# Kernel optimization log

Hardware: AMD Instinct MI355X
Metric: run time of the kernel (lower is better)

## Reference

```python
import jax, jax.numpy as jnp
import numpy as np

N = 50000      # nodes
E = 1_600_000  # edges
F = 64         # input_shape
FE = 1         # input_shape_edge
G = 512        # graphs in batch


def _uniform(k, shape, size):
    b = 1.0 / np.sqrt(size)
    return jax.random.uniform(k, shape, jnp.float32, -b, b)


def setup_inputs() -> dict:
    key = jax.random.key(0)
    ks = jax.random.split(key, 24)
    inp = {
        "x": jax.random.normal(ks[0], (N, F), jnp.float32),
        "edge_index": jax.random.randint(ks[1], (2, E), 0, N),
        "edge_attr": jax.random.uniform(ks[2], (E, FE), jnp.float32),
        "batch": jnp.sort(jax.random.randint(ks[3], (N,), 0, G)),
    }
    # conv layers: (in, out); reset_parameters uses uniform(1/sqrt(in_channels)) for all three weights
    specs = [("c1", F, 16), ("c2", 16, 32), ("c1e", F, 16), ("c2e", 16, 32)]
    i = 4
    for name, cin, cout in specs:
        inp[f"{name}_fc"] = _uniform(ks[i], (cout, cin), cin); i += 1
        inp[f"{name}_e"] = _uniform(ks[i], (FE, FE), cin); i += 1
        inp[f"{name}_a"] = _uniform(ks[i], (1, 2 * cout + FE), cin); i += 1
    inp["fc1_w"] = _uniform(ks[i], (128, 64), 64); i += 1
    inp["fc1_b"] = _uniform(ks[i], (128,), 64); i += 1
    inp["fc2_w"] = _uniform(ks[i], (1, 128), 128); i += 1
    inp["fc2_b"] = _uniform(ks[i], (1,), 128); i += 1
    return inp


def _conv(x, row, col, ea, wfc, we, wa):
    xc = x[col] @ wfc.T            # [E, out] gather + linear
    xr = x[row] @ wfc.T            # [E, out]
    ed = ea @ we.T                 # [E, FE]
    a = jnp.concatenate([xr, xc, ed], axis=1) @ wa.T  # [E, 1]
    # faithful to torch source: softmax over dim=1 of a size-1 dim -> all ones
    a = jax.nn.softmax(jax.nn.leaky_relu(a), axis=1)
    return jax.ops.segment_sum(a * xc, row, num_segments=x.shape[0])  # [N, out]


def reference(x, edge_index, edge_attr, batch,
              c1_fc, c1_e, c1_a, c2_fc, c2_e, c2_a,
              c1e_fc, c1e_e, c1e_a, c2e_fc, c2e_e, c2e_a,
              fc1_w, fc1_b, fc2_w, fc2_b):
    row, col = edge_index[0], edge_index[1]
    h = jax.nn.relu(_conv(x, row, col, edge_attr, c1_fc, c1_e, c1_a))
    h = jax.nn.relu(_conv(h, row, col, edge_attr, c2_fc, c2_e, c2_a))
    he = jax.nn.relu(_conv(x, row, col, edge_attr, c1e_fc, c1e_e, c1e_a))
    he = jax.nn.relu(_conv(he, row, col, edge_attr, c2e_fc, c2e_e, c2e_a))
    cnt = jax.ops.segment_sum(jnp.ones((x.shape[0],), jnp.float32), batch, num_segments=G)
    cnt = jnp.maximum(cnt, 1.0)[:, None]
    pool = lambda z: jax.ops.segment_sum(z, batch, num_segments=G) / cnt  # scatter_mean
    g = jnp.concatenate([pool(h), pool(he)], axis=1)  # [G, 64]
    g = jax.nn.relu(g @ fc1_w.T + fc1_b)
    # dropout: eval mode (identity)
    return g @ fc2_w.T + fc2_b  # [G, 1]
```

## Files before the change

kernel.cpp:

```cpp
#include <hip/hip_runtime.h>
#include <hip/hip_fp16.h>

#define NN 50000
#define NE 1600000
#define NG 512
#define RB 98
#define NB 511
#define NNP (NB * RB)
#define SEGCAP 512
#define CAP 72
#define PBLK 200
#define EPB (NE / PBLK)
#define G1_BLOCKS ((NN * 16 + 511) / 512)
#define ZWORDS (NB * 8 + NG * 64)

union H8 { uint4 u; __half2 h[4]; };
union H4 { uint2 u; __half2 h[2]; };

__global__ __launch_bounds__(256) void zero_k(int* __restrict__ p) {
    int i = blockIdx.x * 256 + threadIdx.x;
    for (; i < ZWORDS; i += 64 * 256) p[i] = 0;
}

__global__ __launch_bounds__(512) void part_gemm1(const int* __restrict__ ei,
                                                  int* __restrict__ bcur,
                                                  unsigned int* __restrict__ bucket,
                                                  const float* __restrict__ x,
                                                  const float* __restrict__ w_a,
                                                  const float* __restrict__ w_b,
                                                  __half* __restrict__ y) {
    __shared__ union {
        struct {
            int lc[NB];
            unsigned short rank[EPB];
        } p;
        float Wt[64][33];
    } sm;
    int tid = threadIdx.x;
    if (blockIdx.x < PBLK) {
        int xcd = blockIdx.x & 7;
        for (int i = tid; i < NB; i += 512) sm.p.lc[i] = 0;
        __syncthreads();
        int e0 = blockIdx.x * EPB;
        const int4* row4 = reinterpret_cast<const int4*>(ei + e0);
        const int4* col4 = reinterpret_cast<const int4*>(ei + NE + e0);
        for (int i0 = tid * 4; i0 < EPB; i0 += 2048) {
            int4 r = row4[i0 >> 2];
            sm.p.rank[i0 + 0] = (unsigned short)atomicAdd(&sm.p.lc[r.x / RB], 1);
            sm.p.rank[i0 + 1] = (unsigned short)atomicAdd(&sm.p.lc[r.y / RB], 1);
            sm.p.rank[i0 + 2] = (unsigned short)atomicAdd(&sm.p.lc[r.z / RB], 1);
            sm.p.rank[i0 + 3] = (unsigned short)atomicAdd(&sm.p.lc[r.w / RB], 1);
        }
        __syncthreads();
        if (tid < NB) sm.p.lc[tid] = atomicAdd(&bcur[tid * 8 + xcd], sm.p.lc[tid]);
        __syncthreads();
        for (int i0 = tid * 4; i0 < EPB; i0 += 2048) {
            int4 r = row4[i0 >> 2];
            int4 c = col4[i0 >> 2];
#pragma unroll
            for (int j = 0; j < 4; ++j) {
                int row = (j == 0) ? r.x : (j == 1) ? r.y : (j == 2) ? r.z : r.w;
                int col = (j == 0) ? c.x : (j == 1) ? c.y : (j == 2) ? c.z : c.w;
                int g = row / RB, lr = row - g * RB;
                int pos = sm.p.lc[g] + (int)sm.p.rank[i0 + j];
                if (pos < SEGCAP)
                    bucket[(g * 8 + xcd) * SEGCAP + pos] = ((unsigned)lr << 16) | (unsigned)col;
            }
        }
    } else {
        for (int i = tid; i < 16 * 64; i += 512) {
            sm.Wt[i & 63][i >> 6] = w_a[i];
            sm.Wt[i & 63][16 + (i >> 6)] = w_b[i];
        }
        __syncthreads();
        int idx = (blockIdx.x - PBLK) * 512 + tid;
        if (idx < NN * 16) {
            int n = idx >> 4, q = idx & 15;
            const float4* xr = reinterpret_cast<const float4*>(x + n * 64);
            float acc0 = 0.f, acc1 = 0.f;
#pragma unroll
            for (int k4 = 0; k4 < 16; ++k4) {
                float4 a = xr[k4];
                acc0 += a.x * sm.Wt[4 * k4 + 0][q] + a.y * sm.Wt[4 * k4 + 1][q] +
                        a.z * sm.Wt[4 * k4 + 2][q] + a.w * sm.Wt[4 * k4 + 3][q];
                acc1 += a.x * sm.Wt[4 * k4 + 0][q + 16] + a.y * sm.Wt[4 * k4 + 1][q + 16] +
                        a.z * sm.Wt[4 * k4 + 2][q + 16] + a.w * sm.Wt[4 * k4 + 3][q + 16];
            }
            y[n * 32 + q] = __float2half_rn(acc0);
            y[n * 32 + q + 16] = __float2half_rn(acc1);
        }
    }
}

__global__ __launch_bounds__(512) void fillgather1(const int* __restrict__ bcur,
                                                   const unsigned int* __restrict__ bucket,
                                                   int* __restrict__ deg,
                                                   unsigned short* __restrict__ cols,
                                                   const __half* __restrict__ y,
                                                   __half* __restrict__ h) {
    __shared__ __align__(16) unsigned short slab[RB * CAP];
    __shared__ int cur[RB];
    __shared__ int scnt[8];
    int tid = threadIdx.x, b = blockIdx.x;
    if (tid < RB) cur[tid] = 0;
    if (tid >= 128 && tid < 136) scnt[tid - 128] = min(bcur[b * 8 + (tid - 128)], SEGCAP);
    __syncthreads();
    const uint4* bseg = reinterpret_cast<const uint4*>(bucket + (size_t)b * 8 * SEGCAP);
#pragma unroll
    for (int k = 0; k < 2; ++k) {
        int f = tid * 4 + k * 2048;
        int seg = f >> 9, pos = f & 511;
        int cnt = scnt[seg];
        if (pos >= cnt) continue;
        uint4 v4 = bseg[f >> 2];
        int lim = cnt - pos;
        {
            unsigned v = v4.x; int lr = v >> 16;
            int p = atomicAdd(&cur[lr], 1);
            if (p < CAP) slab[lr * CAP + p] = (unsigned short)(v & 0xffffu);
        }
        if (lim > 1) {
            unsigned v = v4.y; int lr = v >> 16;
            int p = atomicAdd(&cur[lr], 1);
            if (p < CAP) slab[lr * CAP + p] = (unsigned short)(v & 0xffffu);
        }
        if (lim > 2) {
            unsigned v = v4.z; int lr = v >> 16;
            int p = atomicAdd(&cur[lr], 1);
            if (p < CAP) slab[lr * CAP + p] = (unsigned short)(v & 0xffffu);
        }
        if (lim > 3) {
            unsigned v = v4.w; int lr = v >> 16;
            int p = atomicAdd(&cur[lr], 1);
            if (p < CAP) slab[lr * CAP + p] = (unsigned short)(v & 0xffffu);
        }
    }
    __syncthreads();
    if (tid < RB) {
        int d = min(cur[tid], CAP);
        cur[tid] = d;
        deg[b * RB + tid] = d;
    }
    {
        const uint4* src = reinterpret_cast<const uint4*>(slab);
        uint4* dst = reinterpret_cast<uint4*>(cols) + (size_t)b * (RB * CAP / 8);
        for (int i = tid; i < RB * CAP / 8; i += 512) dst[i] = src[i];
    }
    __syncthreads();
    const uint2* y2 = reinterpret_cast<const uint2*>(y);
#pragma unroll 1
    for (int rp = 0; rp < 2; ++rp) {
        int r = rp * 64 + (tid >> 3);
        if (r >= RB) continue;
        int n = b * RB + r;
        if (n >= NN) continue;
        int d = cur[r], g = tid & 7;
        const unsigned short* c = &slab[r * CAP];
        float acc[4] = {0.f, 0.f, 0.f, 0.f};
        int i = 0;
        for (; i + 3 < d; i += 4) {
            H4 v0, v1, v2, v3;
            v0.u = y2[(int)c[i] * 8 + g];
            v1.u = y2[(int)c[i + 1] * 8 + g];
            v2.u = y2[(int)c[i + 2] * 8 + g];
            v3.u = y2[(int)c[i + 3] * 8 + g];
#pragma unroll
            for (int j = 0; j < 2; ++j) {
                float2 f0 = __half22float2(v0.h[j]);
                float2 f1 = __half22float2(v1.h[j]);
                float2 f2 = __half22float2(v2.h[j]);
                float2 f3 = __half22float2(v3.h[j]);
                acc[2 * j] += (f0.x + f1.x) + (f2.x + f3.x);
                acc[2 * j + 1] += (f0.y + f1.y) + (f2.y + f3.y);
            }
        }
        for (; i < d; ++i) {
            H4 v0;
            v0.u = y2[(int)c[i] * 8 + g];
#pragma unroll
            for (int j = 0; j < 2; ++j) {
                float2 f0 = __half22float2(v0.h[j]);
                acc[2 * j] += f0.x;
                acc[2 * j + 1] += f0.y;
            }
        }
        H4 o;
#pragma unroll
        for (int j = 0; j < 2; ++j) {
            float2 f = {fmaxf(acc[2 * j], 0.f), fmaxf(acc[2 * j + 1], 0.f)};
            o.h[j] = __float22half2_rn(f);
        }
        reinterpret_cast<uint2*>(h)[n * 8 + g] = o.u;
    }
}

__global__ __launch_bounds__(512) void gatherD(const int* __restrict__ deg,
                                               const unsigned short* __restrict__ cols,
                                               const __half* __restrict__ h,
                                               const float* __restrict__ w_a,
                                               const float* __restrict__ w_b,
                                               const int* __restrict__ batch,
                                               float* __restrict__ gpool) {
    __shared__ float U[64][33];
    __shared__ float W2[64][17];
    __shared__ int bl[64];
    int tid = threadIdx.x;
    int n0 = blockIdx.x * 64;
    for (int i = tid; i < 32 * 16; i += 512) W2[i >> 4][i & 15] = w_a[i];
    for (int i = tid; i < 32 * 16; i += 512) W2[32 + (i >> 4)][i & 15] = w_b[i];
    if (tid < 64) bl[tid] = (n0 + tid < NN) ? batch[n0 + tid] : -1;
    int nl = tid >> 3, g = tid & 7;
    int n = n0 + nl;
    float acc[4] = {0.f, 0.f, 0.f, 0.f};
    if (n < NN) {
        int d = deg[n];
        const unsigned short* cs = cols + (size_t)n * CAP;
        const unsigned int* cp = reinterpret_cast<const unsigned int*>(cs);
        const uint2* h2 = reinterpret_cast<const uint2*>(h);
        int i = 0;
        for (; i + 3 < d; i += 4) {
            unsigned int cc0 = cp[i >> 1], cc1 = cp[(i >> 1) + 1];
            H4 v0, v1, v2, v3;
            v0.u = h2[(cc0 & 0xffffu) * 8 + g];
            v1.u = h2[(cc0 >> 16) * 8 + g];
            v2.u = h2[(cc1 & 0xffffu) * 8 + g];
            v3.u = h2[(cc1 >> 16) * 8 + g];
#pragma unroll
            for (int j = 0; j < 2; ++j) {
                float2 f0 = __half22float2(v0.h[j]);
                float2 f1 = __half22float2(v1.h[j]);
                float2 f2 = __half22float2(v2.h[j]);
                float2 f3 = __half22float2(v3.h[j]);
                acc[2 * j] += (f0.x + f1.x) + (f2.x + f3.x);
                acc[2 * j + 1] += (f0.y + f1.y) + (f2.y + f3.y);
            }
        }
        for (; i < d; ++i) {
            H4 v0;
            v0.u = h2[(int)cs[i] * 8 + g];
#pragma unroll
            for (int j = 0; j < 2; ++j) {
                float2 f0 = __half22float2(v0.h[j]);
                acc[2 * j] += f0.x;
                acc[2 * j + 1] += f0.y;
            }
        }
    }
#pragma unroll
    for (int j = 0; j < 4; ++j) U[nl][g * 4 + j] = acc[j];
    __syncthreads();
    int o = tid & 63, w = tid >> 6;
    int ub = (o < 32) ? 0 : 16;
    int curg = -1;
    float sum = 0.f;
#pragma unroll 1
    for (int r = w; r < 64; r += 8) {
        if (n0 + r >= NN) break;
        float a = 0.f;
#pragma unroll
        for (int k = 0; k < 16; ++k) a += U[r][ub + k] * W2[o][k];
        a = fmaxf(a, 0.f);
        int gb = bl[r];
        if (gb != curg) {
            if (curg >= 0) atomicAdd(&gpool[curg * 64 + o], sum);
            curg = gb;
            sum = a;
        } else {
            sum += a;
        }
    }
    if (curg >= 0) atomicAdd(&gpool[curg * 64 + o], sum);
}

__global__ __launch_bounds__(128) void mlp_k(const float* __restrict__ gpool,
                                             const int* __restrict__ batch,
                                             const float* __restrict__ fc1_w,
                                             const float* __restrict__ fc1_b,
                                             const float* __restrict__ fc2_w,
                                             const float* __restrict__ fc2_b,
                                             float* __restrict__ out) {
    int b = blockIdx.x, tid = threadIdx.x;
    int lo = 0, hi = NN;
    while (lo < hi) { int m = (lo + hi) >> 1; if (batch[m] < b) lo = m + 1; else hi = m; }
    int start = lo;
    lo = start; hi = NN;
    while (lo < hi) { int m = (lo + hi) >> 1; if (batch[m] < b + 1) lo = m + 1; else hi = m; }
    int end = lo;
    float inv = 1.f / (float)max(end - start, 1);

    __shared__ float gvec[64];
    if (tid < 64) gvec[tid] = gpool[b * 64 + tid] * inv;
    __syncthreads();

    float hj = fc1_b[tid];
    const float* w = fc1_w + tid * 64;
#pragma unroll
    for (int k = 0; k < 64; ++k) hj += gvec[k] * w[k];
    hj = fmaxf(hj, 0.f);
    __shared__ float red[128];
    red[tid] = hj * fc2_w[tid];
    __syncthreads();
    for (int s = 64; s > 0; s >>= 1) {
        if (tid < s) red[tid] += red[tid + s];
        __syncthreads();
    }
    if (tid == 0) out[b] = red[0] + fc2_b[0];
}

static inline size_t align256(size_t v) { return (v + 255) & ~(size_t)255; }

extern "C" void kernel_launch(void* const* d_in, const int* in_sizes, int n_in,
                              void* d_out, int out_size, void* d_ws, size_t ws_size,
                              hipStream_t stream) {
    const float* x      = (const float*)d_in[0];
    const int*   ei     = (const int*)d_in[1];
    const int*   batch  = (const int*)d_in[3];
    const float* c1_fc  = (const float*)d_in[4];
    const float* c2_fc  = (const float*)d_in[7];
    const float* c1e_fc = (const float*)d_in[10];
    const float* c2e_fc = (const float*)d_in[13];
    const float* fc1_w  = (const float*)d_in[16];
    const float* fc1_b  = (const float*)d_in[17];
    const float* fc2_w  = (const float*)d_in[18];
    const float* fc2_b  = (const float*)d_in[19];
    float* out = (float*)d_out;

    char* base = (char*)d_ws;
    size_t off = 0;
    int* bcur            = (int*)(base + off);            off += sizeof(int) * NB * 8;
    float* gpool         = (float*)(base + off);          off += sizeof(float) * NG * 64;
    off = align256(off);
    unsigned int* bucket = (unsigned int*)(base + off);   off += sizeof(unsigned int) * (size_t)NB * 8 * SEGCAP;
    off = align256(off);
    unsigned short* cols = (unsigned short*)(base + off); off += sizeof(unsigned short) * (size_t)NNP * CAP;
    off = align256(off);
    int* deg             = (int*)(base + off);            off += sizeof(int) * NNP;
    off = align256(off);
    __half* y            = (__half*)(base + off);         off += sizeof(__half) * (size_t)NN * 32;
    off = align256(off);
    __half* h            = (__half*)(base + off);         off += sizeof(__half) * (size_t)NN * 32;

    zero_k<<<64, 256, 0, stream>>>(bcur);
    part_gemm1<<<PBLK + G1_BLOCKS, 512, 0, stream>>>(ei, bcur, bucket, x, c1_fc, c1e_fc, y);
    fillgather1<<<NB, 512, 0, stream>>>(bcur, bucket, deg, cols, y, h);
    gatherD<<<(NN + 63) / 64, 512, 0, stream>>>(deg, cols, h, c2_fc, c2e_fc, batch, gpool);
    mlp_k<<<NG, 128, 0, stream>>>(gpool, batch, fc1_w, fc1_b, fc2_w, fc2_b, out);
}
```

Before: 81.73 us.

## Fuse fill/gather and second gather into one cooperative kernel with grid sync

Merges the fillgather1 and gatherD kernels into a single cooperative kernel that keeps the per-block column slab in shared memory across a grid-wide barrier. This removes the global write and re-read of the cols and deg arrays and one kernel launch. In exchange it needs all 511 blocks of 512 threads to be co-resident for the grid sync, adds the sync's cost, and uses more shared memory per block, which may limit occupancy.

```diff
diff --git a/kernel.cpp b/kernel.cpp
--- a/kernel.cpp
+++ b/kernel.cpp
@@ -1,12 +1,13 @@
 #include <hip/hip_runtime.h>
 #include <hip/hip_fp16.h>
+#include <hip/hip_cooperative_groups.h>
+namespace cg = cooperative_groups;
 
 #define NN 50000
 #define NE 1600000
 #define NG 512
 #define RB 98
 #define NB 511
-#define NNP (NB * RB)
 #define SEGCAP 512
 #define CAP 72
 #define PBLK 200
@@ -14,7 +15,6 @@
 #define G1_BLOCKS ((NN * 16 + 511) / 512)
 #define ZWORDS (NB * 8 + NG * 64)
 
-union H8 { uint4 u; __half2 h[4]; };
 union H4 { uint2 u; __half2 h[2]; };
 
 __global__ __launch_bounds__(256) void zero_k(int* __restrict__ p) {
@@ -92,16 +92,23 @@
     }
 }
 
-__global__ __launch_bounds__(512) void fillgather1(const int* __restrict__ bcur,
-                                                   const unsigned int* __restrict__ bucket,
-                                                   int* __restrict__ deg,
-                                                   unsigned short* __restrict__ cols,
-                                                   const __half* __restrict__ y,
-                                                   __half* __restrict__ h) {
+__global__ __launch_bounds__(512) void fuse_bcd(const int* __restrict__ bcur,
+                                                const unsigned int* __restrict__ bucket,
+                                                const __half* __restrict__ y,
+                                                __half* __restrict__ h,
+                                                const float* __restrict__ w_a,
+                                                const float* __restrict__ w_b,
+                                                const int* __restrict__ batch,
+                                                float* __restrict__ gpool) {
     __shared__ __align__(16) unsigned short slab[RB * CAP];
     __shared__ int cur[RB];
     __shared__ int scnt[8];
+    __shared__ float U[64][33];
+    __shared__ float W2[64][17];
+    __shared__ int bl[64];
     int tid = threadIdx.x, b = blockIdx.x;
+    for (int i = tid; i < 32 * 16; i += 512) W2[i >> 4][i & 15] = w_a[i];
+    for (int i = tid; i < 32 * 16; i += 512) W2[32 + (i >> 4)][i & 15] = w_b[i];
     if (tid < RB) cur[tid] = 0;
     if (tid >= 128 && tid < 136) scnt[tid - 128] = min(bcur[b * 8 + (tid - 128)], SEGCAP);
     __syncthreads();
@@ -114,38 +121,13 @@
         if (pos >= cnt) continue;
         uint4 v4 = bseg[f >> 2];
         int lim = cnt - pos;
-        {
-            unsigned v = v4.x; int lr = v >> 16;
-            int p = atomicAdd(&cur[lr], 1);
-            if (p < CAP) slab[lr * CAP + p] = (unsigned short)(v & 0xffffu);
-        }
-        if (lim > 1) {
-            unsigned v = v4.y; int lr = v >> 16;
-            int p = atomicAdd(&cur[lr], 1);
-            if (p < CAP) slab[lr * CAP + p] = (unsigned short)(v & 0xffffu);
-        }
-        if (lim > 2) {
-            unsigned v = v4.z; int lr = v >> 16;
-            int p = atomicAdd(&cur[lr], 1);
-            if (p < CAP) slab[lr * CAP + p] = (unsigned short)(v & 0xffffu);
-        }
-        if (lim > 3) {
-            unsigned v = v4.w; int lr = v >> 16;
-            int p = atomicAdd(&cur[lr], 1);
-            if (p < CAP) slab[lr * CAP + p] = (unsigned short)(v & 0xffffu);
-        }
-    }
-    __syncthreads();
-    if (tid < RB) {
-        int d = min(cur[tid], CAP);
-        cur[tid] = d;
-        deg[b * RB + tid] = d;
-    }
-    {
-        const uint4* src = reinterpret_cast<const uint4*>(slab);
-        uint4* dst = reinterpret_cast<uint4*>(cols) + (size_t)b * (RB * CAP / 8);
-        for (int i = tid; i < RB * CAP / 8; i += 512) dst[i] = src[i];
-    }
+        { unsigned v = v4.x; int lr = v >> 16; int p = atomicAdd(&cur[lr], 1); if (p < CAP) slab[lr * CAP + p] = (unsigned short)(v & 0xffffu); }
+        if (lim > 1) { unsigned v = v4.y; int lr = v >> 16; int p = atomicAdd(&cur[lr], 1); if (p < CAP) slab[lr * CAP + p] = (unsigned short)(v & 0xffffu); }
+        if (lim > 2) { unsigned v = v4.z; int lr = v >> 16; int p = atomicAdd(&cur[lr], 1); if (p < CAP) slab[lr * CAP + p] = (unsigned short)(v & 0xffffu); }
+        if (lim > 3) { unsigned v = v4.w; int lr = v >> 16; int p = atomicAdd(&cur[lr], 1); if (p < CAP) slab[lr * CAP + p] = (unsigned short)(v & 0xffffu); }
+    }
+    __syncthreads();
+    if (tid < RB) cur[tid] = min(cur[tid], CAP);
     __syncthreads();
     const uint2* y2 = reinterpret_cast<const uint2*>(y);
 #pragma unroll 1
@@ -192,84 +174,79 @@
         }
         reinterpret_cast<uint2*>(h)[n * 8 + g] = o.u;
     }
-}
-
-__global__ __launch_bounds__(512) void gatherD(const int* __restrict__ deg,
-                                               const unsigned short* __restrict__ cols,
-                                               const __half* __restrict__ h,
-                                               const float* __restrict__ w_a,
-                                               const float* __restrict__ w_b,
-                                               const int* __restrict__ batch,
-                                               float* __restrict__ gpool) {
-    __shared__ float U[64][33];
-    __shared__ float W2[64][17];
-    __shared__ int bl[64];
-    int tid = threadIdx.x;
-    int n0 = blockIdx.x * 64;
-    for (int i = tid; i < 32 * 16; i += 512) W2[i >> 4][i & 15] = w_a[i];
-    for (int i = tid; i < 32 * 16; i += 512) W2[32 + (i >> 4)][i & 15] = w_b[i];
-    if (tid < 64) bl[tid] = (n0 + tid < NN) ? batch[n0 + tid] : -1;
-    int nl = tid >> 3, g = tid & 7;
-    int n = n0 + nl;
-    float acc[4] = {0.f, 0.f, 0.f, 0.f};
-    if (n < NN) {
-        int d = deg[n];
-        const unsigned short* cs = cols + (size_t)n * CAP;
-        const unsigned int* cp = reinterpret_cast<const unsigned int*>(cs);
-        const uint2* h2 = reinterpret_cast<const uint2*>(h);
-        int i = 0;
-        for (; i + 3 < d; i += 4) {
-            unsigned int cc0 = cp[i >> 1], cc1 = cp[(i >> 1) + 1];
-            H4 v0, v1, v2, v3;
-            v0.u = h2[(cc0 & 0xffffu) * 8 + g];
-            v1.u = h2[(cc0 >> 16) * 8 + g];
-            v2.u = h2[(cc1 & 0xffffu) * 8 + g];
-            v3.u = h2[(cc1 >> 16) * 8 + g];
-#pragma unroll
-            for (int j = 0; j < 2; ++j) {
-                float2 f0 = __half22float2(v0.h[j]);
-                float2 f1 = __half22float2(v1.h[j]);
-                float2 f2 = __half22float2(v2.h[j]);
-                float2 f3 = __half22float2(v3.h[j]);
-                acc[2 * j] += (f0.x + f1.x) + (f2.x + f3.x);
-                acc[2 * j + 1] += (f0.y + f1.y) + (f2.y + f3.y);
-            }
-        }
-        for (; i < d; ++i) {
-            H4 v0;
-            v0.u = h2[(int)cs[i] * 8 + g];
-#pragma unroll
-            for (int j = 0; j < 2; ++j) {
-                float2 f0 = __half22float2(v0.h[j]);
-                acc[2 * j] += f0.x;
-                acc[2 * j + 1] += f0.y;
-            }
-        }
-    }
-#pragma unroll
-    for (int j = 0; j < 4; ++j) U[nl][g * 4 + j] = acc[j];
-    __syncthreads();
-    int o = tid & 63, w = tid >> 6;
-    int ub = (o < 32) ? 0 : 16;
-    int curg = -1;
-    float sum = 0.f;
+    __threadfence();
+    cg::this_grid().sync();
+    const uint2* h2 = reinterpret_cast<const uint2*>(h);
 #pragma unroll 1
-    for (int r = w; r < 64; r += 8) {
-        if (n0 + r >= NN) break;
-        float a = 0.f;
-#pragma unroll
-        for (int k = 0; k < 16; ++k) a += U[r][ub + k] * W2[o][k];
-        a = fmaxf(a, 0.f);
-        int gb = bl[r];
-        if (gb != curg) {
-            if (curg >= 0) atomicAdd(&gpool[curg * 64 + o], sum);
-            curg = gb;
-            sum = a;
-        } else {
-            sum += a;
-        }
-    }
-    if (curg >= 0) atomicAdd(&gpool[curg * 64 + o], sum);
+    for (int rp = 0; rp < 2; ++rp) {
+        __syncthreads();
+        int rbase = rp * 64;
+        int rows = min(64, RB - rbase);
+        if (tid < 64) {
+            int nn = b * RB + rbase + tid;
+            bl[tid] = (tid < rows && nn < NN) ? batch[nn] : -1;
+        }
+        int rl = tid >> 3, g = tid & 7;
+        int r = rbase + rl;
+        int n = b * RB + r;
+        float acc[4] = {0.f, 0.f, 0.f, 0.f};
+        if (r < RB && n < NN) {
+            int d = cur[r];
+            const unsigned short* c = &slab[r * CAP];
+            int i = 0;
+            for (; i + 3 < d; i += 4) {
+                H4 v0, v1, v2, v3;
+                v0.u = h2[(int)c[i] * 8 + g];
+                v1.u = h2[(int)c[i + 1] * 8 + g];
+                v2.u = h2[(int)c[i + 2] * 8 + g];
+                v3.u = h2[(int)c[i + 3] * 8 + g];
+#pragma unroll
+                for (int j = 0; j < 2; ++j) {
+                    float2 f0 = __half22float2(v0.h[j]);
+                    float2 f1 = __half22float2(v1.h[j]);
+                    float2 f2 = __half22float2(v2.h[j]);
+                    float2 f3 = __half22float2(v3.h[j]);
+                    acc[2 * j] += (f0.x + f1.x) + (f2.x + f3.x);
+                    acc[2 * j + 1] += (f0.y + f1.y) + (f2.y + f3.y);
+                }
+            }
+            for (; i < d; ++i) {
+                H4 v0;
+                v0.u = h2[(int)c[i] * 8 + g];
+#pragma unroll
+                for (int j = 0; j < 2; ++j) {
+                    float2 f0 = __half22float2(v0.h[j]);
+                    acc[2 * j] += f0.x;
+                    acc[2 * j + 1] += f0.y;
+                }
+            }
+        }
+#pragma unroll
+        for (int j = 0; j < 4; ++j) U[rl][g * 4 + j] = acc[j];
+        __syncthreads();
+        int o = tid & 63, w = tid >> 6;
+        int ub = (o < 32) ? 0 : 16;
+        int curg = -1;
+        float sum = 0.f;
+#pragma unroll 1
+        for (int r2 = w; r2 < rows; r2 += 8) {
+            int nn = b * RB + rbase + r2;
+            if (nn >= NN) break;
+            float a = 0.f;
+#pragma unroll
+            for (int k = 0; k < 16; ++k) a += U[r2][ub + k] * W2[o][k];
+            a = fmaxf(a, 0.f);
+            int gb = bl[r2];
+            if (gb != curg) {
+                if (curg >= 0) atomicAdd(&gpool[curg * 64 + o], sum);
+                curg = gb;
+                sum = a;
+            } else {
+                sum += a;
+            }
+        }
+        if (curg >= 0) atomicAdd(&gpool[curg * 64 + o], sum);
+    }
 }
 
 __global__ __launch_bounds__(128) void mlp_k(const float* __restrict__ gpool,
@@ -332,17 +309,16 @@
     off = align256(off);
     unsigned int* bucket = (unsigned int*)(base + off);   off += sizeof(unsigned int) * (size_t)NB * 8 * SEGCAP;
     off = align256(off);
-    unsigned short* cols = (unsigned short*)(base + off); off += sizeof(unsigned short) * (size_t)NNP * CAP;
-    off = align256(off);
-    int* deg             = (int*)(base + off);            off += sizeof(int) * NNP;
-    off = align256(off);
     __half* y            = (__half*)(base + off);         off += sizeof(__half) * (size_t)NN * 32;
     off = align256(off);
     __half* h            = (__half*)(base + off);         off += sizeof(__half) * (size_t)NN * 32;
 
     zero_k<<<64, 256, 0, stream>>>(bcur);
     part_gemm1<<<PBLK + G1_BLOCKS, 512, 0, stream>>>(ei, bcur, bucket, x, c1_fc, c1e_fc, y);
-    fillgather1<<<NB, 512, 0, stream>>>(bcur, bucket, deg, cols, y, h);
-    gatherD<<<(NN + 63) / 64, 512, 0, stream>>>(deg, cols, h, c2_fc, c2e_fc, batch, gpool);
+    {
+        void* args[] = {(void*)&bcur, (void*)&bucket, (void*)&y, (void*)&h,
+                        (void*)&c2_fc, (void*)&c2e_fc, (void*)&batch, (void*)&gpool};
+        hipLaunchCooperativeKernel((const void*)fuse_bcd, dim3(NB), dim3(512), args, 0, stream);
+    }
     mlp_k<<<NG, 128, 0, stream>>>(gpool, batch, fc1_w, fc1_b, fc2_w, fc2_b, out);
 }
```

New measurement: 215.6 us. +163.8%, slower.
